# Performance work log

Hardware: AMD Instinct MI355X
Metric: run time of the kernel (lower is better)

## Reference

```python
import jax, jax.numpy as jnp
import numpy as np

TEMPERATURE = 10.0
CE_WEIGHT = 10.0
NUM_CLUSTERS = 32  # clusters per batch element, labels in [0, K)


def setup_inputs() -> dict:
    key = jax.random.key(0)
    k1, k2, k3, k4, k5 = jax.random.split(key, 5)
    B, N, D, C, K = 4, 2048, 2, 64, NUM_CLUSTERS
    embedding = jax.random.normal(k1, (B, N, D), dtype=jnp.float32)
    contr_emb = jax.random.normal(k2, (B, N, C), dtype=jnp.float32)
    abs_coords = jax.random.normal(k3, (B, N, D), dtype=jnp.float32)
    patch_mask = jax.random.randint(k4, (B, N, N), 0, 2, dtype=jnp.int32)
    cluster_labels = jax.random.randint(k5, (B, N), 0, K, dtype=jnp.int32)
    return {
        "embedding": embedding,
        "contr_emb": contr_emb,
        "abs_coords": abs_coords,
        "patch_mask": patch_mask,
        "cluster_labels": cluster_labels,
    }


def reference(embedding, contr_emb, abs_coords, patch_mask, cluster_labels):
    B, N, D = embedding.shape
    C = contr_emb.shape[-1]
    K = NUM_CLUSTERS

    # --- anchor term: pairwise distance + nonlinearity + masked mean ---
    # diff[b,i,j,:] = (e_i - e_j) + (c_i - c_j)
    diff = (embedding[:, :, None] - embedding[:, None]) + (
        abs_coords[:, :, None] - abs_coords[:, None]
    )  # [B,N,N,D]
    dist_sq = jnp.sum(diff * diff, axis=-1)  # norm(2)^2, [B,N,N]
    nonlinear_dist = 1.0 - jnp.exp(-dist_sq / TEMPERATURE)
    m = (patch_mask == 1).astype(nonlinear_dist.dtype)
    loss = jnp.sum(nonlinear_dist * m) / jnp.sum(m)  # masked mean

    # --- contrastive term ---
    # F.normalize(contr_emb, dim=-1)
    norm = jnp.maximum(jnp.linalg.norm(contr_emb, axis=-1, keepdims=True), 1e-12)
    c = contr_emb / norm  # [B,N,C]

    # per-batch cluster means under no_grad (stop_gradient)
    onehot = jax.nn.one_hot(cluster_labels, K, dtype=c.dtype)  # [B,N,K]
    sums = jnp.einsum("bnc,bnk->bkc", c, onehot)  # [B,K,C]
    counts = jnp.maximum(jnp.sum(onehot, axis=1), 1.0)  # [B,K]
    means = jax.lax.stop_gradient(sums / counts[..., None])  # [B,K,C]

    # cat per-batch [C,K] matrices along cluster axis -> [C, B*K]
    cum_mean_clusters = means.reshape(B * K, C).T
    stacked = c.reshape(B * N, C)
    logits = stacked @ cum_mean_clusters  # [B*N, B*K]

    target = cluster_labels.reshape(-1)  # labels as written (no batch offset)
    logp = jax.nn.log_softmax(logits, axis=-1)
    nll = -jnp.take_along_axis(logp, target[:, None].astype(jnp.int32), axis=1)[:, 0]
    bce_loss = jnp.mean(nll)  # all targets >= 0, so no ignore_index hits

    return loss + CE_WEIGHT * bce_loss
```

## Files before the change

kernel.cpp:

```cpp
#include <hip/hip_runtime.h>
#include <math.h>

#define B_ 4
#define N_ 2048
#define C_ 64
#define K_ 32
#define BN_ (B_ * N_)

#define WS_NLL 0
#define WS_INVN 64
#define WS_SX 8320
#define WS_SY 16512
#define WS_MEANS 24704
#define WS_APART 32896

__global__ __launch_bounds__(256) void k_prep(
    const float* __restrict__ emb, const float* __restrict__ absc,
    const float* __restrict__ contr, float* __restrict__ ws) {
  int t = threadIdx.x, lane = t & 63, w = t >> 6;
  int flat = blockIdx.x * 256 + t;
  if (flat == 0) ws[WS_NLL] = 0.0f;
  if (flat < BN_) {
    float2 ev = ((const float2*)emb)[flat];
    float2 av = ((const float2*)absc)[flat];
    ws[WS_SX + flat] = ev.x + av.x;
    ws[WS_SY + flat] = ev.y + av.y;
  }
  int row = blockIdx.x * 4 + w;
  float x = contr[row * C_ + lane];
  float ss = x * x;
#pragma unroll
  for (int off = 32; off > 0; off >>= 1) ss += __shfl_xor(ss, off);
  if (lane == 0) ws[WS_INVN + row] = 1.0f / fmaxf(sqrtf(ss), 1e-12f);
}

__global__ __launch_bounds__(256) void k_cluster(
    const float* __restrict__ contr, const int* __restrict__ labels,
    float* __restrict__ ws) {
  __shared__ int lsLab[N_];
  __shared__ float lsum[4][64];
  __shared__ float lcnt[4];
  int t = threadIdx.x, lane = t & 63, w = t >> 6;
  int b = blockIdx.x >> 5, k = blockIdx.x & 31;
  const int4* lab4 = (const int4*)(labels + b * N_);
  int4* l4 = (int4*)lsLab;
  l4[t] = lab4[t];
  l4[t + 256] = lab4[t + 256];
  __syncthreads();
  float acc = 0.0f, cnt = 0.0f;
  for (int g0 = w * 512; g0 < w * 512 + 512; g0 += 64) {
    unsigned long long mb = __ballot(lsLab[g0 + lane] == k);
    while (mb) {
      int bit = __ffsll((unsigned long long)mb) - 1;
      mb &= mb - 1;
      int r = b * N_ + g0 + bit;
      float inv = ws[WS_INVN + r];
      acc += contr[(size_t)r * C_ + lane] * inv;
      cnt += 1.0f;
    }
  }
  lsum[w][lane] = acc;
  if (lane == 0) lcnt[w] = cnt;
  __syncthreads();
  if (t < 64) {
    float s = lsum[0][t] + lsum[1][t] + lsum[2][t] + lsum[3][t];
    float c = lcnt[0] + lcnt[1] + lcnt[2] + lcnt[3];
    ws[WS_MEANS + (b * K_ + k) * C_ + t] = s / fmaxf(c, 1.0f);
  }
}

__global__ __launch_bounds__(128) void k_logits_nll(
    const float* __restrict__ contr, const int* __restrict__ labels,
    float* __restrict__ ws) {
  __shared__ float lc[32 * C_];
  __shared__ float lm[2][32], lsv[2][32], ltl[32];
  int t = threadIdx.x, lane = t & 63, w = t >> 6;
  int r0 = blockIdx.x * 32;
  int j = w * 64 + lane;
  const float4* mean4 = (const float4*)(ws + WS_MEANS);
  float4 mk[16];
#pragma unroll
  for (int q = 0; q < 16; ++q) mk[q] = mean4[j * 16 + q];
  const float4* c4 = (const float4*)(contr + (size_t)r0 * C_);
  float4* lc4 = (float4*)lc;
  lc4[t] = c4[t];
  lc4[t + 128] = c4[t + 128];
  lc4[t + 256] = c4[t + 256];
  lc4[t + 384] = c4[t + 384];
  __syncthreads();
  for (int r = 0; r < 32; ++r) {
    const float4* cr = lc4 + r * 16;
    float acc = 0.0f;
#pragma unroll
    for (int q = 0; q < 16; ++q) {
      float4 cv = cr[q];
      acc += cv.x * mk[q].x + cv.y * mk[q].y + cv.z * mk[q].z + cv.w * mk[q].w;
    }
    acc *= ws[WS_INVN + r0 + r];
    float m = acc;
#pragma unroll
    for (int off = 32; off > 0; off >>= 1) m = fmaxf(m, __shfl_xor(m, off));
    float s = __expf(acc - m);
#pragma unroll
    for (int off = 32; off > 0; off >>= 1) s += __shfl_xor(s, off);
    int tgt = labels[r0 + r];
    float tl = __shfl(acc, tgt);
    if (lane == 0) {
      lm[w][r] = m;
      lsv[w][r] = s;
      if (w == 0) ltl[r] = tl;
    }
  }
  __syncthreads();
  if (t < 32) {
    float m0 = lm[0][t], m1 = lm[1][t];
    float mm = fmaxf(m0, m1);
    float ss = lsv[0][t] * __expf(m0 - mm) + lsv[1][t] * __expf(m1 - mm);
    float nll = (mm + __logf(ss)) - ltl[t];
#pragma unroll
    for (int off = 16; off > 0; off >>= 1) nll += __shfl_xor(nll, off);
    if (t == 0) atomicAdd(&ws[WS_NLL], nll);
  }
}

__device__ __forceinline__ void pair4(float sx, float sy, float4 xs, float4 ys,
                                      int4 m, float& acc, int& cnt) {
  float dx, dy, d2, v;
  dx = sx - xs.x; dy = sy - ys.x; d2 = dx * dx + dy * dy;
  v = 1.0f - __expf(d2 * -0.1f);
  if (m.x == 1) { acc += v; cnt += 1; }
  dx = sx - xs.y; dy = sy - ys.y; d2 = dx * dx + dy * dy;
  v = 1.0f - __expf(d2 * -0.1f);
  if (m.y == 1) { acc += v; cnt += 1; }
  dx = sx - xs.z; dy = sy - ys.z; d2 = dx * dx + dy * dy;
  v = 1.0f - __expf(d2 * -0.1f);
  if (m.z == 1) { acc += v; cnt += 1; }
  dx = sx - xs.w; dy = sy - ys.w; d2 = dx * dx + dy * dy;
  v = 1.0f - __expf(d2 * -0.1f);
  if (m.w == 1) { acc += v; cnt += 1; }
}

__global__ __launch_bounds__(256) void k_anchor(
    const int* __restrict__ mask, float* __restrict__ ws) {
  __shared__ float red[8];
  int t = threadIdx.x, lane = t & 63, w = t >> 6;
  int flat = blockIdx.x * 256 + t;
  int cg = flat & 511;
  const int4* m4 = (const int4*)mask;
  const float* wsx = ws + WS_SX;
  const float* wsy = ws + WS_SY;
  const float4* sx4 = (const float4*)wsx;
  const float4* sy4 = (const float4*)wsy;
  float acc = 0.0f;
  int cnt = 0;
#pragma unroll
  for (int bt = 0; bt < 4; ++bt) {
    float4 xs = sx4[bt * 512 + cg];
    float4 ys = sy4[bt * 512 + cg];
#pragma unroll
    for (int j = 0; j < 4; ++j) {
      int idx = flat + (bt * 4 + j) * 262144;
      int4 m = m4[idx];
      int row = idx >> 9;
      float rx = wsx[row], ry = wsy[row];
      pair4(rx, ry, xs, ys, m, acc, cnt);
    }
  }
  float cntf = (float)cnt;
#pragma unroll
  for (int off = 32; off > 0; off >>= 1) {
    acc += __shfl_xor(acc, off);
    cntf += __shfl_xor(cntf, off);
  }
  if (lane == 0) { red[w * 2] = acc; red[w * 2 + 1] = cntf; }
  __syncthreads();
  if (t == 0) {
    ws[WS_APART + blockIdx.x * 2 + 0] = red[0] + red[2] + red[4] + red[6];
    ws[WS_APART + blockIdx.x * 2 + 1] = red[1] + red[3] + red[5] + red[7];
  }
}

__global__ __launch_bounds__(256) void k_final(
    const float* __restrict__ ws, float* __restrict__ out) {
  __shared__ float red[8];
  int t = threadIdx.x, lane = t & 63, w = t >> 6;
  float a = 0.0f, c = 0.0f;
  for (int i = t; i < 1024; i += 256) {
    a += ws[WS_APART + i * 2 + 0];
    c += ws[WS_APART + i * 2 + 1];
  }
#pragma unroll
  for (int off = 32; off > 0; off >>= 1) {
    a += __shfl_xor(a, off);
    c += __shfl_xor(c, off);
  }
  if (lane == 0) { red[w * 2] = a; red[w * 2 + 1] = c; }
  __syncthreads();
  if (t == 0) {
    float at = red[0] + red[2] + red[4] + red[6];
    float ct = red[1] + red[3] + red[5] + red[7];
    out[0] = at / ct + 10.0f * ws[WS_NLL] * (1.0f / (float)BN_);
  }
}

extern "C" void kernel_launch(void* const* d_in, const int* in_sizes, int n_in,
                              void* d_out, int out_size, void* d_ws, size_t ws_size,
                              hipStream_t stream) {
  const float* emb    = (const float*)d_in[0];
  const float* contr  = (const float*)d_in[1];
  const float* absc   = (const float*)d_in[2];
  const int*   mask   = (const int*)d_in[3];
  const int*   labels = (const int*)d_in[4];
  float* ws  = (float*)d_ws;
  float* out = (float*)d_out;

  k_prep<<<2048, 256, 0, stream>>>(emb, absc, contr, ws);
  k_cluster<<<B_ * K_, 256, 0, stream>>>(contr, labels, ws);
  k_logits_nll<<<256, 128, 0, stream>>>(contr, labels, ws);
  k_anchor<<<1024, 256, 0, stream>>>(mask, ws);
  k_final<<<1, 256, 0, stream>>>(ws, out);
}
```

Baseline: 146.9 us.

## Fuse five kernels into two with block-role split and last-block final reduction

Merges prep, cluster-mean and anchor work into one launch in which the first 128 blocks compute cluster means and the rest compute the masked anchor sum. Row norms are now recomputed inline instead of staged through workspace, and the anchor blocks build their per-batch coordinate sums in shared memory. The final reduction is folded into the logits kernel using a completion counter and last-block pattern. This removes three launches and the extra global round trips, at the cost of a fence-plus-atomic handoff and some duplicated norm computation.

```diff
diff --git a/kernel.cpp b/kernel.cpp
--- a/kernel.cpp
+++ b/kernel.cpp
@@ -8,72 +8,122 @@
 #define BN_ (B_ * N_)
 
 #define WS_NLL 0
-#define WS_INVN 64
-#define WS_SX 8320
-#define WS_SY 16512
-#define WS_MEANS 24704
-#define WS_APART 32896
-
-__global__ __launch_bounds__(256) void k_prep(
+#define WS_DONE 8
+#define WS_MEANS 64
+#define WS_APART 8320
+
+__device__ __forceinline__ void pair4(float sx, float sy, float4 xs, float4 ys,
+                                      int4 m, float& acc, int& cnt) {
+  float dx, dy, d2, v;
+  dx = sx - xs.x; dy = sy - ys.x; d2 = dx * dx + dy * dy;
+  v = 1.0f - __expf(d2 * -0.1f);
+  if (m.x == 1) { acc += v; cnt += 1; }
+  dx = sx - xs.y; dy = sy - ys.y; d2 = dx * dx + dy * dy;
+  v = 1.0f - __expf(d2 * -0.1f);
+  if (m.y == 1) { acc += v; cnt += 1; }
+  dx = sx - xs.z; dy = sy - ys.z; d2 = dx * dx + dy * dy;
+  v = 1.0f - __expf(d2 * -0.1f);
+  if (m.z == 1) { acc += v; cnt += 1; }
+  dx = sx - xs.w; dy = sy - ys.w; d2 = dx * dx + dy * dy;
+  v = 1.0f - __expf(d2 * -0.1f);
+  if (m.w == 1) { acc += v; cnt += 1; }
+}
+
+__global__ __launch_bounds__(256) void k_main(
     const float* __restrict__ emb, const float* __restrict__ absc,
-    const float* __restrict__ contr, float* __restrict__ ws) {
+    const float* __restrict__ contr, const int* __restrict__ labels,
+    const int* __restrict__ mask, float* __restrict__ ws) {
+  __shared__ union {
+    struct { float sx[N_]; float sy[N_]; } a;
+    struct { int lab[N_]; float lsum[4][64]; float lcnt[4]; } c;
+  } sm;
+  __shared__ float red[8];
   int t = threadIdx.x, lane = t & 63, w = t >> 6;
-  int flat = blockIdx.x * 256 + t;
-  if (flat == 0) ws[WS_NLL] = 0.0f;
-  if (flat < BN_) {
-    float2 ev = ((const float2*)emb)[flat];
-    float2 av = ((const float2*)absc)[flat];
-    ws[WS_SX + flat] = ev.x + av.x;
-    ws[WS_SY + flat] = ev.y + av.y;
-  }
-  int row = blockIdx.x * 4 + w;
-  float x = contr[row * C_ + lane];
-  float ss = x * x;
-#pragma unroll
-  for (int off = 32; off > 0; off >>= 1) ss += __shfl_xor(ss, off);
-  if (lane == 0) ws[WS_INVN + row] = 1.0f / fmaxf(sqrtf(ss), 1e-12f);
-}
-
-__global__ __launch_bounds__(256) void k_cluster(
+  int bid = blockIdx.x;
+  if (bid < 128) {
+    int b = bid >> 5, k = bid & 31;
+    if (bid == 0 && t == 0) {
+      ws[WS_NLL] = 0.0f;
+      ((unsigned*)ws)[WS_DONE] = 0u;
+    }
+    const int4* lab4 = (const int4*)(labels + b * N_);
+    int4* l4 = (int4*)sm.c.lab;
+    l4[t] = lab4[t];
+    l4[t + 256] = lab4[t + 256];
+    __syncthreads();
+    float acc = 0.0f, cnt = 0.0f;
+    for (int g0 = w * 512; g0 < w * 512 + 512; g0 += 64) {
+      unsigned long long mb = __ballot(sm.c.lab[g0 + lane] == k);
+      while (mb) {
+        int bit = __ffsll(mb) - 1;
+        mb &= mb - 1;
+        int r = g0 + bit;
+        float x = contr[(size_t)(b * N_ + r) * C_ + lane];
+        float ss = x * x;
+#pragma unroll
+        for (int off = 32; off > 0; off >>= 1) ss += __shfl_xor(ss, off);
+        acc += x * (1.0f / fmaxf(sqrtf(ss), 1e-12f));
+        cnt += 1.0f;
+      }
+    }
+    sm.c.lsum[w][lane] = acc;
+    if (lane == 0) sm.c.lcnt[w] = cnt;
+    __syncthreads();
+    if (t < 64) {
+      float s = sm.c.lsum[0][t] + sm.c.lsum[1][t] + sm.c.lsum[2][t] + sm.c.lsum[3][t];
+      float c = sm.c.lcnt[0] + sm.c.lcnt[1] + sm.c.lcnt[2] + sm.c.lcnt[3];
+      ws[WS_MEANS + (b * K_ + k) * C_ + t] = s / fmaxf(c, 1.0f);
+    }
+  } else {
+    int aid = bid - 128;
+    int b = aid >> 8;
+    int flat = (aid & 255) * 256 + t;
+    const float4* e4 = (const float4*)(emb + b * N_ * 2);
+    const float4* a4 = (const float4*)(absc + b * N_ * 2);
+    for (int i = t; i < N_ / 2; i += 256) {
+      float4 ev = e4[i], av = a4[i];
+      sm.a.sx[2 * i]     = ev.x + av.x;
+      sm.a.sy[2 * i]     = ev.y + av.y;
+      sm.a.sx[2 * i + 1] = ev.z + av.z;
+      sm.a.sy[2 * i + 1] = ev.w + av.w;
+    }
+    __syncthreads();
+    int cg = flat & 511;
+    float4 xs = ((const float4*)sm.a.sx)[cg];
+    float4 ys = ((const float4*)sm.a.sy)[cg];
+    const int4* m4 = (const int4*)mask + (size_t)b * (N_ * (size_t)N_ / 4);
+    float acc = 0.0f;
+    int cnt = 0;
+#pragma unroll
+    for (int it = 0; it < 16; ++it) {
+      int idx = flat + it * 65536;
+      int4 m = m4[idx];
+      int row = idx >> 9;
+      pair4(sm.a.sx[row], sm.a.sy[row], xs, ys, m, acc, cnt);
+    }
+    float cntf = (float)cnt;
+#pragma unroll
+    for (int off = 32; off > 0; off >>= 1) {
+      acc += __shfl_xor(acc, off);
+      cntf += __shfl_xor(cntf, off);
+    }
+    if (lane == 0) { red[w * 2] = acc; red[w * 2 + 1] = cntf; }
+    __syncthreads();
+    if (t == 0) {
+      ws[WS_APART + aid * 2 + 0] = red[0] + red[2] + red[4] + red[6];
+      ws[WS_APART + aid * 2 + 1] = red[1] + red[3] + red[5] + red[7];
+    }
+  }
+}
+
+__global__ __launch_bounds__(128) void k_logits_final(
     const float* __restrict__ contr, const int* __restrict__ labels,
-    float* __restrict__ ws) {
-  __shared__ int lsLab[N_];
-  __shared__ float lsum[4][64];
-  __shared__ float lcnt[4];
-  int t = threadIdx.x, lane = t & 63, w = t >> 6;
-  int b = blockIdx.x >> 5, k = blockIdx.x & 31;
-  const int4* lab4 = (const int4*)(labels + b * N_);
-  int4* l4 = (int4*)lsLab;
-  l4[t] = lab4[t];
-  l4[t + 256] = lab4[t + 256];
-  __syncthreads();
-  float acc = 0.0f, cnt = 0.0f;
-  for (int g0 = w * 512; g0 < w * 512 + 512; g0 += 64) {
-    unsigned long long mb = __ballot(lsLab[g0 + lane] == k);
-    while (mb) {
-      int bit = __ffsll((unsigned long long)mb) - 1;
-      mb &= mb - 1;
-      int r = b * N_ + g0 + bit;
-      float inv = ws[WS_INVN + r];
-      acc += contr[(size_t)r * C_ + lane] * inv;
-      cnt += 1.0f;
-    }
-  }
-  lsum[w][lane] = acc;
-  if (lane == 0) lcnt[w] = cnt;
-  __syncthreads();
-  if (t < 64) {
-    float s = lsum[0][t] + lsum[1][t] + lsum[2][t] + lsum[3][t];
-    float c = lcnt[0] + lcnt[1] + lcnt[2] + lcnt[3];
-    ws[WS_MEANS + (b * K_ + k) * C_ + t] = s / fmaxf(c, 1.0f);
-  }
-}
-
-__global__ __launch_bounds__(128) void k_logits_nll(
-    const float* __restrict__ contr, const int* __restrict__ labels,
-    float* __restrict__ ws) {
+    float* __restrict__ ws, float* __restrict__ out) {
   __shared__ float lc[32 * C_];
+  __shared__ float invr[32];
   __shared__ float lm[2][32], lsv[2][32], ltl[32];
+  __shared__ float fred[4];
+  __shared__ int lastf;
   int t = threadIdx.x, lane = t & 63, w = t >> 6;
   int r0 = blockIdx.x * 32;
   int j = w * 64 + lane;
@@ -88,6 +138,14 @@
   lc4[t + 256] = c4[t + 256];
   lc4[t + 384] = c4[t + 384];
   __syncthreads();
+  for (int r = w * 16; r < w * 16 + 16; ++r) {
+    float x = lc[r * C_ + lane];
+    float ss = x * x;
+#pragma unroll
+    for (int off = 32; off > 0; off >>= 1) ss += __shfl_xor(ss, off);
+    if (lane == 0) invr[r] = 1.0f / fmaxf(sqrtf(ss), 1e-12f);
+  }
+  __syncthreads();
   for (int r = 0; r < 32; ++r) {
     const float4* cr = lc4 + r * 16;
     float acc = 0.0f;
@@ -96,7 +154,7 @@
       float4 cv = cr[q];
       acc += cv.x * mk[q].x + cv.y * mk[q].y + cv.z * mk[q].z + cv.w * mk[q].w;
     }
-    acc *= ws[WS_INVN + r0 + r];
+    acc *= invr[r];
     float m = acc;
 #pragma unroll
     for (int off = 32; off > 0; off >>= 1) m = fmaxf(m, __shfl_xor(m, off));
@@ -121,85 +179,32 @@
     for (int off = 16; off > 0; off >>= 1) nll += __shfl_xor(nll, off);
     if (t == 0) atomicAdd(&ws[WS_NLL], nll);
   }
-}
-
-__device__ __forceinline__ void pair4(float sx, float sy, float4 xs, float4 ys,
-                                      int4 m, float& acc, int& cnt) {
-  float dx, dy, d2, v;
-  dx = sx - xs.x; dy = sy - ys.x; d2 = dx * dx + dy * dy;
-  v = 1.0f - __expf(d2 * -0.1f);
-  if (m.x == 1) { acc += v; cnt += 1; }
-  dx = sx - xs.y; dy = sy - ys.y; d2 = dx * dx + dy * dy;
-  v = 1.0f - __expf(d2 * -0.1f);
-  if (m.y == 1) { acc += v; cnt += 1; }
-  dx = sx - xs.z; dy = sy - ys.z; d2 = dx * dx + dy * dy;
-  v = 1.0f - __expf(d2 * -0.1f);
-  if (m.z == 1) { acc += v; cnt += 1; }
-  dx = sx - xs.w; dy = sy - ys.w; d2 = dx * dx + dy * dy;
-  v = 1.0f - __expf(d2 * -0.1f);
-  if (m.w == 1) { acc += v; cnt += 1; }
-}
-
-__global__ __launch_bounds__(256) void k_anchor(
-    const int* __restrict__ mask, float* __restrict__ ws) {
-  __shared__ float red[8];
-  int t = threadIdx.x, lane = t & 63, w = t >> 6;
-  int flat = blockIdx.x * 256 + t;
-  int cg = flat & 511;
-  const int4* m4 = (const int4*)mask;
-  const float* wsx = ws + WS_SX;
-  const float* wsy = ws + WS_SY;
-  const float4* sx4 = (const float4*)wsx;
-  const float4* sy4 = (const float4*)wsy;
-  float acc = 0.0f;
-  int cnt = 0;
-#pragma unroll
-  for (int bt = 0; bt < 4; ++bt) {
-    float4 xs = sx4[bt * 512 + cg];
-    float4 ys = sy4[bt * 512 + cg];
-#pragma unroll
-    for (int j = 0; j < 4; ++j) {
-      int idx = flat + (bt * 4 + j) * 262144;
-      int4 m = m4[idx];
-      int row = idx >> 9;
-      float rx = wsx[row], ry = wsy[row];
-      pair4(rx, ry, xs, ys, m, acc, cnt);
-    }
-  }
-  float cntf = (float)cnt;
-#pragma unroll
-  for (int off = 32; off > 0; off >>= 1) {
-    acc += __shfl_xor(acc, off);
-    cntf += __shfl_xor(cntf, off);
-  }
-  if (lane == 0) { red[w * 2] = acc; red[w * 2 + 1] = cntf; }
   __syncthreads();
   if (t == 0) {
-    ws[WS_APART + blockIdx.x * 2 + 0] = red[0] + red[2] + red[4] + red[6];
-    ws[WS_APART + blockIdx.x * 2 + 1] = red[1] + red[3] + red[5] + red[7];
-  }
-}
-
-__global__ __launch_bounds__(256) void k_final(
-    const float* __restrict__ ws, float* __restrict__ out) {
-  __shared__ float red[8];
-  int t = threadIdx.x, lane = t & 63, w = t >> 6;
-  float a = 0.0f, c = 0.0f;
-  for (int i = t; i < 1024; i += 256) {
-    a += ws[WS_APART + i * 2 + 0];
-    c += ws[WS_APART + i * 2 + 1];
-  }
-#pragma unroll
-  for (int off = 32; off > 0; off >>= 1) {
-    a += __shfl_xor(a, off);
-    c += __shfl_xor(c, off);
-  }
-  if (lane == 0) { red[w * 2] = a; red[w * 2 + 1] = c; }
-  __syncthreads();
-  if (t == 0) {
-    float at = red[0] + red[2] + red[4] + red[6];
-    float ct = red[1] + red[3] + red[5] + red[7];
-    out[0] = at / ct + 10.0f * ws[WS_NLL] * (1.0f / (float)BN_);
+    __threadfence();
+    unsigned v = atomicAdd(&((unsigned*)ws)[WS_DONE], 1u);
+    lastf = (v == 255u);
+  }
+  __syncthreads();
+  if (lastf) {
+    __threadfence();
+    float a = 0.0f, c = 0.0f;
+    for (int i = t; i < 1024; i += 128) {
+      a += ws[WS_APART + i * 2 + 0];
+      c += ws[WS_APART + i * 2 + 1];
+    }
+#pragma unroll
+    for (int off = 32; off > 0; off >>= 1) {
+      a += __shfl_xor(a, off);
+      c += __shfl_xor(c, off);
+    }
+    if (lane == 0) { fred[w * 2] = a; fred[w * 2 + 1] = c; }
+    __syncthreads();
+    if (t == 0) {
+      float at = fred[0] + fred[2];
+      float ct = fred[1] + fred[3];
+      out[0] = at / ct + 10.0f * ws[WS_NLL] * (1.0f / (float)BN_);
+    }
   }
 }
 
@@ -214,9 +219,6 @@
   float* ws  = (float*)d_ws;
   float* out = (float*)d_out;
 
-  k_prep<<<2048, 256, 0, stream>>>(emb, absc, contr, ws);
-  k_cluster<<<B_ * K_, 256, 0, stream>>>(contr, labels, ws);
-  k_logits_nll<<<256, 128, 0, stream>>>(contr, labels, ws);
-  k_anchor<<<1024, 256, 0, stream>>>(mask, ws);
-  k_final<<<1, 256, 0, stream>>>(ws, out);
-}
+  k_main<<<128 + 1024, 256, 0, stream>>>(emb, absc, contr, labels, mask, ws);
+  k_logits_final<<<256, 128, 0, stream>>>(contr, labels, ws, out);
+}
```

After: 154.8 us. +5.4%, slower.
